# Kernel optimization log

Measured on AMD Instinct MI355X. Metric: run time of the kernel, lower is better.

## Reference

```python
import jax, jax.numpy as jnp
import numpy as np

PATCH = 7
STRIDE = 1
PDIM = 3 * PATCH * PATCH  # 147


def _extract_patches(im):
    # torch.nn.Unfold(kernel=7, stride=1): output [b, c*k*k, L] with channel-major
    # ordering, which matches conv_general_dilated_patches' channel-major layout.
    b = im.shape[0]
    p = jax.lax.conv_general_dilated_patches(
        im, filter_shape=(PATCH, PATCH), window_strides=(STRIDE, STRIDE), padding='VALID'
    )  # [b, 147, h', w']
    p = p.reshape(b, PDIM, -1).transpose(0, 2, 1)  # [b, L, 147]
    # normalize_patch='mean': std_mean over ALL dims, only the mean is subtracted
    return p - p.mean()


def setup_inputs() -> dict:
    key = jax.random.key(0)
    k1, k2, k3, k4, k5 = jax.random.split(key, 5)
    B, C, H, W = 16, 3, 128, 128
    L = ((H - PATCH) // STRIDE + 1) ** 2  # 14884
    n_samples, n_proj = 4096, 128
    x = jax.random.normal(k1, (B, C, H, W), dtype=jnp.float32)
    y = jax.random.normal(k2, (B, C, H, W), dtype=jnp.float32)
    # faithful quirk: sample_same_locations=True re-draws a fresh permutation for y
    idx_x = jax.random.permutation(k3, L)[:n_samples].astype(jnp.int32)
    idx_y = jax.random.permutation(k4, L)[:n_samples].astype(jnp.int32)
    proj = jax.random.normal(k5, (PDIM, n_proj), dtype=jnp.float32)
    proj = proj / jnp.linalg.norm(proj, axis=0, keepdims=True)  # unit-norm slices
    return {"x": x, "y": y, "proj": proj, "idx_x": idx_x, "idx_y": idx_y}


def reference(x, y, proj, idx_x, idx_y):
    xp = _extract_patches(x)[:, idx_x]  # [b, n, 147]
    yp = _extract_patches(y)[:, idx_y]  # [b, n, 147]
    # SWD dist_metric, vectorized over the batch dim (replaces the Python loop):
    # project patches onto random unit directions, sort along the sample axis,
    # mean absolute difference of sorted projections.
    px = jnp.sort(jnp.einsum('bnd,dp->bnp', xp, proj), axis=1)  # [b, n, P]
    py = jnp.sort(jnp.einsum('bnd,dp->bnp', yp, proj), axis=1)
    per_sample = jnp.mean(jnp.abs(px - py), axis=(1, 2))  # [b]
    return per_sample.mean()  # batch_reduction='mean'
```

## Files before the change

kernel.cpp:

```cpp
#include <hip/hip_runtime.h>
#include <cstddef>
#include <cstdint>

#define BATCH 16
#define CHAN 3
#define HH 128
#define WW 128
#define PATCHK 7
#define HP 122
#define PDIM 147
#define NSAMP 4096
#define NPROJ 128
#define IMG_PIX (CHAN*HH*WW)
#define TOT_PIX (BATCH*IMG_PIX)
#define COUNT_D ((double)BATCH*HP*HP*PDIM)

__global__ __launch_bounds__(256)
void k_wsum(const float* __restrict__ x, const float* __restrict__ y,
            double* __restrict__ outx, double* __restrict__ outy) {
  float sx = 0.f, sy = 0.f;
  const int stride = gridDim.x * blockDim.x;
  for (int e = blockIdx.x * blockDim.x + threadIdx.x; e < TOT_PIX; e += stride) {
    int j = e & (WW - 1);
    int i = (e >> 7) & (HH - 1);
    int wi = min(i, HP - 1) - max(0, i - (PATCHK - 1)) + 1;
    int wj = min(j, HP - 1) - max(0, j - (PATCHK - 1)) + 1;
    float w = (float)(wi * wj);
    sx = fmaf(x[e], w, sx);
    sy = fmaf(y[e], w, sy);
  }
  __shared__ float rx[256], ry[256];
  const int tid = threadIdx.x;
  rx[tid] = sx; ry[tid] = sy;
  __syncthreads();
  for (int off = 128; off; off >>= 1) {
    if (tid < off) { rx[tid] += rx[tid + off]; ry[tid] += ry[tid + off]; }
    __syncthreads();
  }
  if (tid == 0) { outx[blockIdx.x] = (double)rx[0]; outy[blockIdx.x] = (double)ry[0]; }
}

__global__ void k_meandiff(const double* __restrict__ px, const double* __restrict__ py,
                           double* __restrict__ dmean,
                           const float* __restrict__ proj, float* __restrict__ sp) {
  const int tid = threadIdx.x;
  if (tid < NPROJ) {
    float s = 0.f;
    for (int d = 0; d < PDIM; ++d) s += proj[d * NPROJ + tid];
    sp[tid] = s;
  }
  __shared__ double sd[256];
  sd[tid] = px[tid] - py[tid];
  __syncthreads();
  for (int off = 128; off; off >>= 1) {
    if (tid < off) sd[tid] += sd[tid + off];
    __syncthreads();
  }
  if (tid == 0) dmean[0] = sd[0] / COUNT_D;
}

#define TM 128
#define ASTR (TM + 2)
#define KROWS 74
#define MINK(v) ((v) < 146 ? (v) : 146)

#define LB(dst, kk) _Pragma("unroll") \
  for (int pp = 0; pp < 16; ++pp) dst[pp] = bpr[(kk) * NPROJ + pp];

#define FMAK(kk, bb) { \
  const float2 a_ = *(const float2*)&As[(kk) * ASTR + lane * 2]; \
  _Pragma("unroll") \
  for (int pp = 0; pp < 16; ++pp) { \
    acc0[pp] = fmaf(a_.x, bb[pp], acc0[pp]); \
    acc1[pp] = fmaf(a_.y, bb[pp], acc1[pp]); } }

__global__ __launch_bounds__(512, 8)
void k_proj(const float* __restrict__ x, const float* __restrict__ y,
            const float* __restrict__ proj,
            const int* __restrict__ idx_x, const int* __restrict__ idx_y,
            float* __restrict__ PX, float* __restrict__ PY) {
  __shared__ float As[KROWS * ASTR];
  __shared__ int offd[PDIM];
  __shared__ int basen[TM];

  const int z = blockIdx.z;
  const float* im = z ? y : x;
  const int* idx = z ? idx_y : idx_x;
  float* dst = z ? PY : PX;
  const int b = blockIdx.y;
  const int nbase = blockIdx.x * TM;
  const int tid = threadIdx.x;

  if (tid < PDIM) {
    int c = tid / 49, r = tid - c * 49, kh = r / 7, kw = r - kh * 7;
    offd[tid] = (c * HH + kh) * WW + kw;
  }
  if (tid >= 256 && tid < 256 + TM) {
    int n = tid - 256;
    int l = idx[nbase + n];
    int h0 = l / HP;
    basen[n] = h0 * WW + (l - h0 * HP);
  }
  __syncthreads();

  const float* imb = im + b * IMG_PIX;
  const int lane = tid & 63;
  const int w = __builtin_amdgcn_readfirstlane(tid >> 6);
  const float* bpr = proj + w * 16;

  float acc0[16], acc1[16];
#pragma unroll
  for (int pp = 0; pp < 16; ++pp) { acc0[pp] = 0.f; acc1[pp] = 0.f; }

#pragma unroll 1
  for (int ph = 0; ph < 2; ++ph) {
    const int k0 = ph ? KROWS : 0;
    if (ph) __syncthreads();

    for (int e = tid; e < KROWS * TM; e += 512) {
      int n = e / KROWS;
      int dr = e - n * KROWS;
      int d = dr + k0;
      As[dr * ASTR + n] = (d < PDIM) ? imb[basen[n] + offd[d]] : 0.f;
    }
    __syncthreads();

    float b0[16], b1[16], b2[16], b3[16];
    LB(b0, k0); LB(b1, k0 + 1); LB(b2, k0 + 2);
    for (int kk = 0; kk < 72; kk += 4) {
      LB(b3, MINK(k0 + kk + 3));
      FMAK(kk, b0);
      LB(b0, MINK(k0 + kk + 4));
      FMAK(kk + 1, b1);
      LB(b1, MINK(k0 + kk + 5));
      FMAK(kk + 2, b2);
      LB(b2, MINK(k0 + kk + 6));
      FMAK(kk + 3, b3);
    }
    FMAK(72, b0);
    FMAK(73, b1);
  }

#pragma unroll
  for (int pp = 0; pp < 16; ++pp) {
    float* o = dst + (size_t)(b * NPROJ + w * 16 + pp) * NSAMP + nbase + lane * 2;
    *(float2*)o = make_float2(acc0[pp], acc1[pp]);
  }
}

__device__ __forceinline__ float xorf(float v, unsigned m) {
  return __int_as_float(__float_as_int(v) ^ (int)m);
}
#define CSW(a, b) { float _t = fminf(a, b); b = fmaxf(a, b); a = _t; }

#define SORT8A(v) do { \
  CSW(v[0],v[1]); CSW(v[3],v[2]); CSW(v[4],v[5]); CSW(v[7],v[6]); \
  CSW(v[0],v[2]); CSW(v[1],v[3]); CSW(v[6],v[4]); CSW(v[7],v[5]); \
  CSW(v[0],v[1]); CSW(v[2],v[3]); CSW(v[5],v[4]); CSW(v[7],v[6]); \
  CSW(v[0],v[4]); CSW(v[1],v[5]); CSW(v[2],v[6]); CSW(v[3],v[7]); \
  CSW(v[0],v[2]); CSW(v[1],v[3]); CSW(v[4],v[6]); CSW(v[5],v[7]); \
  CSW(v[0],v[1]); CSW(v[2],v[3]); CSW(v[4],v[5]); CSW(v[6],v[7]); } while (0)

#define REG3A(v) do { \
  CSW(v[0],v[4]); CSW(v[1],v[5]); CSW(v[2],v[6]); CSW(v[3],v[7]); \
  CSW(v[0],v[2]); CSW(v[1],v[3]); CSW(v[4],v[6]); CSW(v[5],v[7]); \
  CSW(v[0],v[1]); CSW(v[2],v[3]); CSW(v[4],v[5]); CSW(v[6],v[7]); } while (0)

#define FLIP8(v, m) { v[0]=xorf(v[0],m); v[1]=xorf(v[1],m); v[2]=xorf(v[2],m); \
  v[3]=xorf(v[3],m); v[4]=xorf(v[4],m); v[5]=xorf(v[5],m); v[6]=xorf(v[6],m); \
  v[7]=xorf(v[7],m); }

template <int DL>
__device__ __forceinline__ float swzxor(float v) {
  if constexpr (DL == 1) {
    return __int_as_float(
        __builtin_amdgcn_mov_dpp(__float_as_int(v), 0xB1, 0xF, 0xF, true));
  } else if constexpr (DL == 2) {
    return __int_as_float(
        __builtin_amdgcn_mov_dpp(__float_as_int(v), 0x4E, 0xF, 0xF, true));
  } else if constexpr (DL <= 16) {
    return __int_as_float(
        __builtin_amdgcn_ds_swizzle(__float_as_int(v), (DL << 10) | 0x1F));
  } else {
    return __shfl_xor(v, DL, 64);
  }
}

template <int DL>
__device__ __forceinline__ void shufxy(float (&vx)[8], float (&vy)[8], bool keepLo) {
#pragma unroll
  for (int r = 0; r < 8; ++r) {
    float ox = swzxor<DL>(vx[r]);
    vx[r] = keepLo ? fminf(vx[r], ox) : fmaxf(vx[r], ox);
    float oy = swzxor<DL>(vy[r]);
    vy[r] = keepLo ? fminf(vy[r], oy) : fmaxf(vy[r], oy);
  }
}

__device__ __forceinline__ void lds_stage(float (&vx)[8], float (&vy)[8],
                                          float* lx, float* ly, int t, int dl, bool kl) {
  ((float4*)lx)[t * 2]     = make_float4(vx[0], vx[1], vx[2], vx[3]);
  ((float4*)lx)[t * 2 + 1] = make_float4(vx[4], vx[5], vx[6], vx[7]);
  ((float4*)ly)[t * 2]     = make_float4(vy[0], vy[1], vy[2], vy[3]);
  ((float4*)ly)[t * 2 + 1] = make_float4(vy[4], vy[5], vy[6], vy[7]);
  __syncthreads();
  const int pt = (t ^ dl) * 2;
  float4 ox0 = ((const float4*)lx)[pt], ox1 = ((const float4*)lx)[pt + 1];
  float4 oy0 = ((const float4*)ly)[pt], oy1 = ((const float4*)ly)[pt + 1];
  vx[0] = kl ? fminf(vx[0], ox0.x) : fmaxf(vx[0], ox0.x);
  vx[1] = kl ? fminf(vx[1], ox0.y) : fmaxf(vx[1], ox0.y);
  vx[2] = kl ? fminf(vx[2], ox0.z) : fmaxf(vx[2], ox0.z);
  vx[3] = kl ? fminf(vx[3], ox0.w) : fmaxf(vx[3], ox0.w);
  vx[4] = kl ? fminf(vx[4], ox1.x) : fmaxf(vx[4], ox1.x);
  vx[5] = kl ? fminf(vx[5], ox1.y) : fmaxf(vx[5], ox1.y);
  vx[6] = kl ? fminf(vx[6], ox1.z) : fmaxf(vx[6], ox1.z);
  vx[7] = kl ? fminf(vx[7], ox1.w) : fmaxf(vx[7], ox1.w);
  vy[0] = kl ? fminf(vy[0], oy0.x) : fmaxf(vy[0], oy0.x);
  vy[1] = kl ? fminf(vy[1], oy0.y) : fmaxf(vy[1], oy0.y);
  vy[2] = kl ? fminf(vy[2], oy0.z) : fmaxf(vy[2], oy0.z);
  vy[3] = kl ? fminf(vy[3], oy0.w) : fmaxf(vy[3], oy0.w);
  vy[4] = kl ? fminf(vy[4], oy1.x) : fmaxf(vy[4], oy1.x);
  vy[5] = kl ? fminf(vy[5], oy1.y) : fmaxf(vy[5], oy1.y);
  vy[6] = kl ? fminf(vy[6], oy1.z) : fmaxf(vy[6], oy1.z);
  vy[7] = kl ? fminf(vy[7], oy1.w) : fmaxf(vy[7], oy1.w);
  __syncthreads();
}

__global__ __launch_bounds__(512)
void k_sortdiff(const float* __restrict__ PX, const float* __restrict__ PY,
                const float* __restrict__ sp, const double* __restrict__ dmean,
                float* __restrict__ bsum) {
  __shared__ float lx[NSAMP];
  __shared__ float ly[NSAMP];
  __shared__ float red[8];
  const int bp = blockIdx.x;
  const int p = bp & (NPROJ - 1);
  const unsigned t = threadIdx.x;

  const unsigned g = t ^ (t >> 1);
  const unsigned mA    = (t & 1u)   << 31;
  const unsigned dA16  = (g & 1u)   << 31;
  const unsigned d16   = (g & 2u)   << 30;
  const unsigned d32   = (g & 4u)   << 29;
  const unsigned d64   = (g & 8u)   << 28;
  const unsigned d128  = (g & 16u)  << 27;
  const unsigned d256  = (g & 32u)  << 26;
  const unsigned d512  = (g & 64u)  << 25;
  const unsigned d1024 = (g & 128u) << 24;
  const unsigned d2048 = (t & 256u) << 23;

  const bool k1  = (t & 1u)  == 0, k2  = (t & 2u)  == 0, k4 = (t & 4u) == 0;
  const bool k8  = (t & 8u)  == 0, k16 = (t & 16u) == 0, k32 = (t & 32u) == 0;
  const bool kl64 = (t & 64u) == 0, kl128 = (t & 128u) == 0, kl256 = (t & 256u) == 0;

  float vx[8], vy[8];
  {
    const float4* rx = (const float4*)(PX + (size_t)bp * NSAMP) + t * 2;
    const float4* ry = (const float4*)(PY + (size_t)bp * NSAMP) + t * 2;
    float4 x0 = rx[0], x1 = rx[1], y0 = ry[0], y1 = ry[1];
    vx[0]=x0.x; vx[1]=x0.y; vx[2]=x0.z; vx[3]=x0.w;
    vx[4]=x1.x; vx[5]=x1.y; vx[6]=x1.z; vx[7]=x1.w;
    vy[0]=y0.x; vy[1]=y0.y; vy[2]=y0.z; vy[3]=y0.w;
    vy[4]=y1.x; vy[5]=y1.y; vy[6]=y1.z; vy[7]=y1.w;
  }

  FLIP8(vx, mA); FLIP8(vy, mA);
  SORT8A(vx); SORT8A(vy);
  FLIP8(vx, dA16); FLIP8(vy, dA16);

  shufxy<1>(vx, vy, k1); REG3A(vx); REG3A(vy);
  FLIP8(vx, d16); FLIP8(vy, d16);
  shufxy<2>(vx, vy, k2); shufxy<1>(vx, vy, k1); REG3A(vx); REG3A(vy);
  FLIP8(vx, d32); FLIP8(vy, d32);
  shufxy<4>(vx, vy, k4); shufxy<2>(vx, vy, k2); shufxy<1>(vx, vy, k1);
  REG3A(vx); REG3A(vy);
  FLIP8(vx, d64); FLIP8(vy, d64);
  shufxy<8>(vx, vy, k8); shufxy<4>(vx, vy, k4); shufxy<2>(vx, vy, k2);
  shufxy<1>(vx, vy, k1); REG3A(vx); REG3A(vy);
  FLIP8(vx, d128); FLIP8(vy, d128);
  shufxy<16>(vx, vy, k16); shufxy<8>(vx, vy, k8); shufxy<4>(vx, vy, k4);
  shufxy<2>(vx, vy, k2); shufxy<1>(vx, vy, k1); REG3A(vx); REG3A(vy);
  FLIP8(vx, d256); FLIP8(vy, d256);
  shufxy<32>(vx, vy, k32); shufxy<16>(vx, vy, k16); shufxy<8>(vx, vy, k8);
  shufxy<4>(vx, vy, k4); shufxy<2>(vx, vy, k2); shufxy<1>(vx, vy, k1);
  REG3A(vx); REG3A(vy);
  FLIP8(vx, d512); FLIP8(vy, d512);
  lds_stage(vx, vy, lx, ly, (int)t, 64, kl64);
  shufxy<32>(vx, vy, k32); shufxy<16>(vx, vy, k16); shufxy<8>(vx, vy, k8);
  shufxy<4>(vx, vy, k4); shufxy<2>(vx, vy, k2); shufxy<1>(vx, vy, k1);
  REG3A(vx); REG3A(vy);
  FLIP8(vx, d1024); FLIP8(vy, d1024);
  lds_stage(vx, vy, lx, ly, (int)t, 128, kl128);
  lds_stage(vx, vy, lx, ly, (int)t, 64, kl64);
  shufxy<32>(vx, vy, k32); shufxy<16>(vx, vy, k16); shufxy<8>(vx, vy, k8);
  shufxy<4>(vx, vy, k4); shufxy<2>(vx, vy, k2); shufxy<1>(vx, vy, k1);
  REG3A(vx); REG3A(vy);
  FLIP8(vx, d2048); FLIP8(vy, d2048);
  lds_stage(vx, vy, lx, ly, (int)t, 256, kl256);
  lds_stage(vx, vy, lx, ly, (int)t, 128, kl128);
  lds_stage(vx, vy, lx, ly, (int)t, 64, kl64);
  shufxy<32>(vx, vy, k32); shufxy<16>(vx, vy, k16); shufxy<8>(vx, vy, k8);
  shufxy<4>(vx, vy, k4); shufxy<2>(vx, vy, k2); shufxy<1>(vx, vy, k1);
  REG3A(vx); REG3A(vy);

  const float delta = (float)(dmean[0]) * sp[p];
  float s = 0.f;
#pragma unroll
  for (int r = 0; r < 8; ++r) s += fabsf(vx[r] - vy[r] - delta);

#pragma unroll
  for (int o = 1; o < 64; o <<= 1) s += __shfl_xor(s, o, 64);
  if ((t & 63u) == 0) red[t >> 6] = s;
  __syncthreads();
  if (t == 0) {
    float tot = 0.f;
#pragma unroll
    for (int i = 0; i < 8; ++i) tot += red[i];
    bsum[bp] = tot;
  }
}

__global__ void k_final(const float* __restrict__ bsum, float* __restrict__ out) {
  __shared__ double s[256];
  const int tid = threadIdx.x;
  double v = 0.0;
  for (int q = tid; q < BATCH * NPROJ; q += 256) v += (double)bsum[q];
  s[tid] = v;
  __syncthreads();
  for (int off = 128; off; off >>= 1) {
    if (tid < off) s[tid] += s[tid + off];
    __syncthreads();
  }
  if (tid == 0) out[0] = (float)(s[0] / ((double)NSAMP * NPROJ * BATCH));
}

extern "C" void kernel_launch(void* const* d_in, const int* in_sizes, int n_in,
                              void* d_out, int out_size, void* d_ws, size_t ws_size,
                              hipStream_t stream) {
  const float* x    = (const float*)d_in[0];
  const float* y    = (const float*)d_in[1];
  const float* proj = (const float*)d_in[2];
  const int* idx_x  = (const int*)d_in[3];
  const int* idx_y  = (const int*)d_in[4];
  float* out = (float*)d_out;

  char* ws = (char*)d_ws;
  double* pAx   = (double*)(ws + 0);
  double* pAy   = (double*)(ws + 2048);
  double* dmean = (double*)(ws + 4096);
  float*  sp    = (float*)(ws + 4160);
  float*  bsum  = (float*)(ws + 8192);
  float*  PX    = (float*)(ws + 16384);
  float*  PY    = PX + (size_t)BATCH * NPROJ * NSAMP;

  const size_t need = 16384 + 2ull * BATCH * NPROJ * NSAMP * sizeof(float);
  if (ws_size < need) return;

  k_wsum    <<<256, 256, 0, stream>>>(x, y, pAx, pAy);
  k_meandiff<<<1, 256, 0, stream>>>(pAx, pAy, dmean, proj, sp);
  k_proj    <<<dim3(NSAMP / TM, BATCH, 2), 512, 0, stream>>>(x, y, proj, idx_x, idx_y, PX, PY);
  k_sortdiff<<<BATCH * NPROJ, 512, 0, stream>>>(PX, PY, sp, dmean, bsum);
  k_final   <<<1, 256, 0, stream>>>(bsum, out);
}
```

Measured before the change: 226.2 us.

## Restructure bitonic sort to 128 threads with 32 elements per thread

The sort kernel drops from 512 threads holding 8 elements each to 128 threads (two wavefronts) holding four groups of 8 per thread. Cross-group merge stages now happen as register compare-swaps, so only one LDS exchange stride between the two wavefronts remains. The LDS writes use an XOR swizzle to avoid bank conflicts. This cuts barriers and LDS traffic per merge stage, at the cost of much higher register pressure per thread and fewer threads per block.

```diff
diff --git a/kernel.cpp b/kernel.cpp
--- a/kernel.cpp
+++ b/kernel.cpp
@@ -148,6 +148,7 @@
   }
 }
 
+#define SIGNB 0x80000000u
 __device__ __forceinline__ float xorf(float v, unsigned m) {
   return __int_as_float(__float_as_int(v) ^ (int)m);
 }
@@ -197,127 +198,127 @@
   }
 }
 
-__device__ __forceinline__ void lds_stage(float (&vx)[8], float (&vy)[8],
-                                          float* lx, float* ly, int t, int dl, bool kl) {
-  ((float4*)lx)[t * 2]     = make_float4(vx[0], vx[1], vx[2], vx[3]);
-  ((float4*)lx)[t * 2 + 1] = make_float4(vx[4], vx[5], vx[6], vx[7]);
-  ((float4*)ly)[t * 2]     = make_float4(vy[0], vy[1], vy[2], vy[3]);
-  ((float4*)ly)[t * 2 + 1] = make_float4(vy[4], vy[5], vy[6], vy[7]);
-  __syncthreads();
-  const int pt = (t ^ dl) * 2;
-  float4 ox0 = ((const float4*)lx)[pt], ox1 = ((const float4*)lx)[pt + 1];
-  float4 oy0 = ((const float4*)ly)[pt], oy1 = ((const float4*)ly)[pt + 1];
-  vx[0] = kl ? fminf(vx[0], ox0.x) : fmaxf(vx[0], ox0.x);
-  vx[1] = kl ? fminf(vx[1], ox0.y) : fmaxf(vx[1], ox0.y);
-  vx[2] = kl ? fminf(vx[2], ox0.z) : fmaxf(vx[2], ox0.z);
-  vx[3] = kl ? fminf(vx[3], ox0.w) : fmaxf(vx[3], ox0.w);
-  vx[4] = kl ? fminf(vx[4], ox1.x) : fmaxf(vx[4], ox1.x);
-  vx[5] = kl ? fminf(vx[5], ox1.y) : fmaxf(vx[5], ox1.y);
-  vx[6] = kl ? fminf(vx[6], ox1.z) : fmaxf(vx[6], ox1.z);
-  vx[7] = kl ? fminf(vx[7], ox1.w) : fmaxf(vx[7], ox1.w);
-  vy[0] = kl ? fminf(vy[0], oy0.x) : fmaxf(vy[0], oy0.x);
-  vy[1] = kl ? fminf(vy[1], oy0.y) : fmaxf(vy[1], oy0.y);
-  vy[2] = kl ? fminf(vy[2], oy0.z) : fmaxf(vy[2], oy0.z);
-  vy[3] = kl ? fminf(vy[3], oy0.w) : fmaxf(vy[3], oy0.w);
-  vy[4] = kl ? fminf(vy[4], oy1.x) : fmaxf(vy[4], oy1.x);
-  vy[5] = kl ? fminf(vy[5], oy1.y) : fmaxf(vy[5], oy1.y);
-  vy[6] = kl ? fminf(vy[6], oy1.z) : fmaxf(vy[6], oy1.z);
-  vy[7] = kl ? fminf(vy[7], oy1.w) : fmaxf(vy[7], oy1.w);
-  __syncthreads();
-}
-
-__global__ __launch_bounds__(512)
+__device__ __forceinline__ void wstage(float (&v)[4][8], float4* buf4,
+                                       int tid, int sw, bool keep) {
+  float4* wp = buf4 + tid * 8;
+#pragma unroll
+  for (int g = 0; g < 4; ++g) {
+    wp[(g * 2) ^ sw]     = make_float4(v[g][0], v[g][1], v[g][2], v[g][3]);
+    wp[(g * 2 + 1) ^ sw] = make_float4(v[g][4], v[g][5], v[g][6], v[g][7]);
+  }
+  __syncthreads();
+  const float4* rp = buf4 + (tid ^ 64) * 8;
+#pragma unroll
+  for (int g = 0; g < 4; ++g) {
+    float4 o0 = rp[(g * 2) ^ sw];
+    float4 o1 = rp[(g * 2 + 1) ^ sw];
+    v[g][0] = keep ? fminf(v[g][0], o0.x) : fmaxf(v[g][0], o0.x);
+    v[g][1] = keep ? fminf(v[g][1], o0.y) : fmaxf(v[g][1], o0.y);
+    v[g][2] = keep ? fminf(v[g][2], o0.z) : fmaxf(v[g][2], o0.z);
+    v[g][3] = keep ? fminf(v[g][3], o0.w) : fmaxf(v[g][3], o0.w);
+    v[g][4] = keep ? fminf(v[g][4], o1.x) : fmaxf(v[g][4], o1.x);
+    v[g][5] = keep ? fminf(v[g][5], o1.y) : fmaxf(v[g][5], o1.y);
+    v[g][6] = keep ? fminf(v[g][6], o1.z) : fmaxf(v[g][6], o1.z);
+    v[g][7] = keep ? fminf(v[g][7], o1.w) : fmaxf(v[g][7], o1.w);
+  }
+  __syncthreads();
+}
+
+#define FLIPALL(m) { FLIP8(vx[0], m); FLIP8(vx[1], m); FLIP8(vx[2], m); FLIP8(vx[3], m); \
+                     FLIP8(vy[0], m); FLIP8(vy[1], m); FLIP8(vy[2], m); FLIP8(vy[3], m); }
+#define FLIP4G(m0, m1, m2, m3) { \
+  FLIP8(vx[0], m0); FLIP8(vx[1], m1); FLIP8(vx[2], m2); FLIP8(vx[3], m3); \
+  FLIP8(vy[0], m0); FLIP8(vy[1], m1); FLIP8(vy[2], m2); FLIP8(vy[3], m3); }
+#define SHUFALL(DL, KP) { shufxy<DL>(vx[0], vy[0], KP); shufxy<DL>(vx[1], vy[1], KP); \
+                          shufxy<DL>(vx[2], vy[2], KP); shufxy<DL>(vx[3], vy[3], KP); }
+#define REG3ALL() { REG3A(vx[0]); REG3A(vx[1]); REG3A(vx[2]); REG3A(vx[3]); \
+                    REG3A(vy[0]); REG3A(vy[1]); REG3A(vy[2]); REG3A(vy[3]); }
+#define REGJ1(v) { _Pragma("unroll") \
+  for (int r = 0; r < 8; ++r) { CSW(v[0][r], v[1][r]); CSW(v[2][r], v[3][r]); } }
+#define REGJ2(v) { _Pragma("unroll") \
+  for (int r = 0; r < 8; ++r) { CSW(v[0][r], v[2][r]); CSW(v[1][r], v[3][r]); } }
+
+__global__ __launch_bounds__(128, 4)
 void k_sortdiff(const float* __restrict__ PX, const float* __restrict__ PY,
                 const float* __restrict__ sp, const double* __restrict__ dmean,
                 float* __restrict__ bsum) {
-  __shared__ float lx[NSAMP];
-  __shared__ float ly[NSAMP];
-  __shared__ float red[8];
+  __shared__ float4 buf4[1024];
+  __shared__ float red[2];
   const int bp = blockIdx.x;
   const int p = bp & (NPROJ - 1);
-  const unsigned t = threadIdx.x;
-
-  const unsigned g = t ^ (t >> 1);
-  const unsigned mA    = (t & 1u)   << 31;
-  const unsigned dA16  = (g & 1u)   << 31;
-  const unsigned d16   = (g & 2u)   << 30;
-  const unsigned d32   = (g & 4u)   << 29;
-  const unsigned d64   = (g & 8u)   << 28;
-  const unsigned d128  = (g & 16u)  << 27;
-  const unsigned d256  = (g & 32u)  << 26;
-  const unsigned d512  = (g & 64u)  << 25;
-  const unsigned d1024 = (g & 128u) << 24;
-  const unsigned d2048 = (t & 256u) << 23;
-
-  const bool k1  = (t & 1u)  == 0, k2  = (t & 2u)  == 0, k4 = (t & 4u) == 0;
-  const bool k8  = (t & 8u)  == 0, k16 = (t & 16u) == 0, k32 = (t & 32u) == 0;
-  const bool kl64 = (t & 64u) == 0, kl128 = (t & 128u) == 0, kl256 = (t & 256u) == 0;
-
-  float vx[8], vy[8];
+  const int tid = threadIdx.x;
+  const int l = tid & 63;
+  const int w = tid >> 6;
+  const int sw = l & 7;
+
+  float vx[4][8], vy[4][8];
   {
-    const float4* rx = (const float4*)(PX + (size_t)bp * NSAMP) + t * 2;
-    const float4* ry = (const float4*)(PY + (size_t)bp * NSAMP) + t * 2;
-    float4 x0 = rx[0], x1 = rx[1], y0 = ry[0], y1 = ry[1];
-    vx[0]=x0.x; vx[1]=x0.y; vx[2]=x0.z; vx[3]=x0.w;
-    vx[4]=x1.x; vx[5]=x1.y; vx[6]=x1.z; vx[7]=x1.w;
-    vy[0]=y0.x; vy[1]=y0.y; vy[2]=y0.z; vy[3]=y0.w;
-    vy[4]=y1.x; vy[5]=y1.y; vy[6]=y1.z; vy[7]=y1.w;
-  }
-
-  FLIP8(vx, mA); FLIP8(vy, mA);
-  SORT8A(vx); SORT8A(vy);
-  FLIP8(vx, dA16); FLIP8(vy, dA16);
-
-  shufxy<1>(vx, vy, k1); REG3A(vx); REG3A(vy);
-  FLIP8(vx, d16); FLIP8(vy, d16);
-  shufxy<2>(vx, vy, k2); shufxy<1>(vx, vy, k1); REG3A(vx); REG3A(vy);
-  FLIP8(vx, d32); FLIP8(vy, d32);
-  shufxy<4>(vx, vy, k4); shufxy<2>(vx, vy, k2); shufxy<1>(vx, vy, k1);
-  REG3A(vx); REG3A(vy);
-  FLIP8(vx, d64); FLIP8(vy, d64);
-  shufxy<8>(vx, vy, k8); shufxy<4>(vx, vy, k4); shufxy<2>(vx, vy, k2);
-  shufxy<1>(vx, vy, k1); REG3A(vx); REG3A(vy);
-  FLIP8(vx, d128); FLIP8(vy, d128);
-  shufxy<16>(vx, vy, k16); shufxy<8>(vx, vy, k8); shufxy<4>(vx, vy, k4);
-  shufxy<2>(vx, vy, k2); shufxy<1>(vx, vy, k1); REG3A(vx); REG3A(vy);
-  FLIP8(vx, d256); FLIP8(vy, d256);
-  shufxy<32>(vx, vy, k32); shufxy<16>(vx, vy, k16); shufxy<8>(vx, vy, k8);
-  shufxy<4>(vx, vy, k4); shufxy<2>(vx, vy, k2); shufxy<1>(vx, vy, k1);
-  REG3A(vx); REG3A(vy);
-  FLIP8(vx, d512); FLIP8(vy, d512);
-  lds_stage(vx, vy, lx, ly, (int)t, 64, kl64);
-  shufxy<32>(vx, vy, k32); shufxy<16>(vx, vy, k16); shufxy<8>(vx, vy, k8);
-  shufxy<4>(vx, vy, k4); shufxy<2>(vx, vy, k2); shufxy<1>(vx, vy, k1);
-  REG3A(vx); REG3A(vy);
-  FLIP8(vx, d1024); FLIP8(vy, d1024);
-  lds_stage(vx, vy, lx, ly, (int)t, 128, kl128);
-  lds_stage(vx, vy, lx, ly, (int)t, 64, kl64);
-  shufxy<32>(vx, vy, k32); shufxy<16>(vx, vy, k16); shufxy<8>(vx, vy, k8);
-  shufxy<4>(vx, vy, k4); shufxy<2>(vx, vy, k2); shufxy<1>(vx, vy, k1);
-  REG3A(vx); REG3A(vy);
-  FLIP8(vx, d2048); FLIP8(vy, d2048);
-  lds_stage(vx, vy, lx, ly, (int)t, 256, kl256);
-  lds_stage(vx, vy, lx, ly, (int)t, 128, kl128);
-  lds_stage(vx, vy, lx, ly, (int)t, 64, kl64);
-  shufxy<32>(vx, vy, k32); shufxy<16>(vx, vy, k16); shufxy<8>(vx, vy, k8);
-  shufxy<4>(vx, vy, k4); shufxy<2>(vx, vy, k2); shufxy<1>(vx, vy, k1);
-  REG3A(vx); REG3A(vy);
+    const float4* rx = (const float4*)(PX + (size_t)bp * NSAMP + w * 512 + l * 8);
+    const float4* ry = (const float4*)(PY + (size_t)bp * NSAMP + w * 512 + l * 8);
+#pragma unroll
+    for (int g = 0; g < 4; ++g) {
+      float4 a0 = rx[g * 256], a1 = rx[g * 256 + 1];
+      vx[g][0]=a0.x; vx[g][1]=a0.y; vx[g][2]=a0.z; vx[g][3]=a0.w;
+      vx[g][4]=a1.x; vx[g][5]=a1.y; vx[g][6]=a1.z; vx[g][7]=a1.w;
+      float4 b0 = ry[g * 256], b1 = ry[g * 256 + 1];
+      vy[g][0]=b0.x; vy[g][1]=b0.y; vy[g][2]=b0.z; vy[g][3]=b0.w;
+      vy[g][4]=b1.x; vy[g][5]=b1.y; vy[g][6]=b1.z; vy[g][7]=b1.w;
+    }
+  }
+
+  const unsigned gl  = (unsigned)(l ^ (l >> 1));
+  const unsigned mA   = (unsigned)(l & 1) << 31;
+  const unsigned d8   = (gl & 1u)  << 31;
+  const unsigned d16  = (gl & 2u)  << 30;
+  const unsigned d32  = (gl & 4u)  << 29;
+  const unsigned d64  = (gl & 8u)  << 28;
+  const unsigned d128 = (gl & 16u) << 27;
+  const unsigned d256 = (unsigned)(((l >> 5) ^ w) & 1) << 31;
+  const unsigned dW   = (unsigned)w << 31;
+  const bool c1 = (l & 1) == 0, c2 = (l & 2) == 0, c4 = (l & 4) == 0;
+  const bool c8 = (l & 8) == 0, c16 = (l & 16) == 0, c32 = (l & 32) == 0;
+  const bool cW = (w == 0);
+
+  FLIPALL(mA);
+  SORT8A(vx[0]); SORT8A(vx[1]); SORT8A(vx[2]); SORT8A(vx[3]);
+  SORT8A(vy[0]); SORT8A(vy[1]); SORT8A(vy[2]); SORT8A(vy[3]);
+  FLIPALL(d8);
+  SHUFALL(1, c1); REG3ALL(); FLIPALL(d16);
+  SHUFALL(2, c2); SHUFALL(1, c1); REG3ALL(); FLIPALL(d32);
+  SHUFALL(4, c4); SHUFALL(2, c2); SHUFALL(1, c1); REG3ALL(); FLIPALL(d64);
+  SHUFALL(8, c8); SHUFALL(4, c4); SHUFALL(2, c2); SHUFALL(1, c1);
+  REG3ALL(); FLIPALL(d128);
+  SHUFALL(16, c16); SHUFALL(8, c8); SHUFALL(4, c4); SHUFALL(2, c2);
+  SHUFALL(1, c1); REG3ALL(); FLIPALL(d256);
+  SHUFALL(32, c32); SHUFALL(16, c16); SHUFALL(8, c8); SHUFALL(4, c4);
+  SHUFALL(2, c2); SHUFALL(1, c1); REG3ALL();
+  FLIP4G(dW, dW ^ SIGNB, dW, dW ^ SIGNB);
+  wstage(vx, buf4, tid, sw, cW); wstage(vy, buf4, tid, sw, cW);
+  SHUFALL(32, c32); SHUFALL(16, c16); SHUFALL(8, c8); SHUFALL(4, c4);
+  SHUFALL(2, c2); SHUFALL(1, c1); REG3ALL();
+  FLIP4G(0u, SIGNB, SIGNB, 0u);
+  REGJ1(vx); REGJ1(vy);
+  wstage(vx, buf4, tid, sw, cW); wstage(vy, buf4, tid, sw, cW);
+  SHUFALL(32, c32); SHUFALL(16, c16); SHUFALL(8, c8); SHUFALL(4, c4);
+  SHUFALL(2, c2); SHUFALL(1, c1); REG3ALL();
+  FLIP4G(0u, 0u, SIGNB, SIGNB);
+  REGJ2(vx); REGJ2(vy); REGJ1(vx); REGJ1(vy);
+  wstage(vx, buf4, tid, sw, cW); wstage(vy, buf4, tid, sw, cW);
+  SHUFALL(32, c32); SHUFALL(16, c16); SHUFALL(8, c8); SHUFALL(4, c4);
+  SHUFALL(2, c2); SHUFALL(1, c1); REG3ALL();
 
   const float delta = (float)(dmean[0]) * sp[p];
   float s = 0.f;
 #pragma unroll
-  for (int r = 0; r < 8; ++r) s += fabsf(vx[r] - vy[r] - delta);
+  for (int g = 0; g < 4; ++g)
+#pragma unroll
+    for (int r = 0; r < 8; ++r) s += fabsf(vx[g][r] - vy[g][r] - delta);
 
 #pragma unroll
   for (int o = 1; o < 64; o <<= 1) s += __shfl_xor(s, o, 64);
-  if ((t & 63u) == 0) red[t >> 6] = s;
-  __syncthreads();
-  if (t == 0) {
-    float tot = 0.f;
-#pragma unroll
-    for (int i = 0; i < 8; ++i) tot += red[i];
-    bsum[bp] = tot;
-  }
+  if (l == 0) red[w] = s;
+  __syncthreads();
+  if (tid == 0) bsum[bp] = red[0] + red[1];
 }
 
 __global__ void k_final(const float* __restrict__ bsum, float* __restrict__ out) {
@@ -359,6 +360,6 @@
   k_wsum    <<<256, 256, 0, stream>>>(x, y, pAx, pAy);
   k_meandiff<<<1, 256, 0, stream>>>(pAx, pAy, dmean, proj, sp);
   k_proj    <<<dim3(NSAMP / TM, BATCH, 2), 512, 0, stream>>>(x, y, proj, idx_x, idx_y, PX, PY);
-  k_sortdiff<<<BATCH * NPROJ, 512, 0, stream>>>(PX, PY, sp, dmean, bsum);
+  k_sortdiff<<<BATCH * NPROJ, 128, 0, stream>>>(PX, PY, sp, dmean, bsum);
   k_final   <<<1, 256, 0, stream>>>(bsum, out);
 }
```

After: 240.4 us, median of 5. 1.06x slower.
